# Performance work log

Hardware: AMD Instinct MI355X
Metric: run time of the kernel (lower is better)

## Reference

```python
import jax, jax.numpy as jnp
import numpy as np

B, N, P, K = 64, 64, 128, 16

def setup_inputs() -> dict:
    key = jax.random.key(0)
    k1, k2, k3, k4 = jax.random.split(key, 4)
    x = jax.random.normal(k1, (B, N, P), dtype=jnp.float32)
    idx = jax.random.randint(k2, (B, P), 0, K)
    x_mask = jax.nn.one_hot(idx, K, dtype=jnp.float32)  # [B, P, K] one-hot
    # xavier_normal_ init for weights [K, N*N]
    std = float(np.sqrt(2.0 / (K + N * N)))
    weights = std * jax.random.normal(k3, (K, N * N), dtype=jnp.float32)
    g = jax.random.uniform(k4, (N * N, N * N), dtype=jnp.float32)
    return {"x": x, "x_mask": x_mask, "weights": weights, "g": g}

def reference(x, x_mask, weights, g):
    b, n, p = x.shape
    wg = jnp.matmul(weights ** 2, g)               # [K, N*N]
    w = jnp.einsum('bpk,km->bpm', x_mask, wg)      # [B, P, N*N]
    ef = jnp.exp(-w.reshape(b, p, n, n))           # [B, P, N, N]
    # torch does x[b].reshape(p, -1, 1): row-major reinterpretation of [N,P] -> [P,N]
    xr = x.reshape(b, p, n)                        # [B, P, N]
    Z = jnp.einsum('bpij,bpj->bi', ef, xr)         # batched matvec, summed over p
    return (Z, w)
```

## Files before the change

### kernel.cpp

```cpp
#include <hip/hip_runtime.h>
#include <hip/hip_bf16.h>


__global__ __launch_bounds__(256) void k_gemm(const float* __restrict__ W,
                                              const float* __restrict__ G,
                                              float* __restrict__ part) {
    __shared__ float buf[8192];
    const int tc  = blockIdx.x & 15;
    const int mg  = blockIdx.x >> 4;
    const int tid = threadIdx.x;
    const int tt  = tid >> 4;
    const int col = tid & 15;
    const int t0  = tc * 256;

#pragma unroll
    for (int k = 0; k < 16; ++k) {
        float v = W[k * 4096 + t0 + tid];
        buf[k * 256 + tid] = v * v;
    }
    __syncthreads();

    const float4* G4 = (const float4*)G;
    const int mq = mg * 16 + col;

    float4 acc[16];
#pragma unroll
    for (int k = 0; k < 16; ++k) acc[k] = make_float4(0.f, 0.f, 0.f, 0.f);

#pragma unroll 8
    for (int i = 0; i < 16; ++i) {
        const int tl = tt * 16 + i;
        const float4 g4 = G4[(size_t)(t0 + tl) * 1024 + mq];
#pragma unroll
        for (int k = 0; k < 16; ++k) {
            const float s = buf[k * 256 + tl];
            acc[k].x = fmaf(s, g4.x, acc[k].x);
            acc[k].y = fmaf(s, g4.y, acc[k].y);
            acc[k].z = fmaf(s, g4.z, acc[k].z);
            acc[k].w = fmaf(s, g4.w, acc[k].w);
        }
    }
    __syncthreads();

    float4* red = (float4*)buf;
    float4* p4  = (float4*)part;
#pragma unroll
    for (int r = 0; r < 2; ++r) {
#pragma unroll
        for (int ks = 0; ks < 8; ++ks)
            red[ks * 256 + tid] = acc[r * 8 + ks];
        __syncthreads();
        if (tid < 128) {
            const int ks = tid >> 4;
            const int c2 = tid & 15;
            float4 s = make_float4(0.f, 0.f, 0.f, 0.f);
#pragma unroll
            for (int t2 = 0; t2 < 16; ++t2) {
                float4 v = red[ks * 256 + t2 * 16 + c2];
                s.x += v.x; s.y += v.y; s.z += v.z; s.w += v.w;
            }
            const int k = r * 8 + ks;
            p4[(size_t)tc * 16384 + (size_t)k * 1024 + mg * 16 + c2] = s;
        }
        __syncthreads();
    }
}

__global__ __launch_bounds__(256) void k_reduce(const float* __restrict__ part,
                                                float* __restrict__ wg,
                                                float* __restrict__ E) {
    const int q = blockIdx.x * 256 + threadIdx.x;
    const float4* p4 = (const float4*)part;
    float4 s = make_float4(0.f, 0.f, 0.f, 0.f);
#pragma unroll
    for (int tc = 0; tc < 16; ++tc) {
        float4 v = p4[(size_t)tc * 16384 + q];
        s.x += v.x; s.y += v.y; s.z += v.z; s.w += v.w;
    }
    ((float4*)wg)[q] = s;
    ((float4*)E)[q] = make_float4(expf(-s.x), expf(-s.y), expf(-s.z), expf(-s.w));
}

__global__ __launch_bounds__(256) void k_wz(const float* __restrict__ x,
                                            const float* __restrict__ xmask,
                                            const float* __restrict__ wg,
                                            const float* __restrict__ E,
                                            float* __restrict__ wout,
                                            float* __restrict__ zout) {
    __shared__ float sw[4][16][64];
    __shared__ int   idx[128];
    __shared__ float zr[16][16];
    const int tid = threadIdx.x;

    if (blockIdx.x < 8192) {
        const int bp = blockIdx.x;
        const float* xm = xmask + (size_t)bp * 16;
        int k = 0;
#pragma unroll
        for (int i = 0; i < 16; ++i) k = (xm[i] > 0.5f) ? i : k;
        const float4* src = (const float4*)(wg + (size_t)k * 4096);
        float4*       dst = (float4*)(wout + (size_t)bp * 4096);
#pragma unroll
        for (int c = 0; c < 4; ++c)
            dst[c * 256 + tid] = src[c * 256 + tid];
        return;
    }

    const int zb = blockIdx.x - 8192;
    const int b  = zb >> 2;
    const int iq = zb & 3;
    const int wv = tid >> 6;
    const int ln = tid & 63;

    if (tid < 128) {
        const float* xm = xmask + ((size_t)b * 128 + tid) * 16;
        int k = 0;
#pragma unroll
        for (int i = 0; i < 16; ++i) k = (xm[i] > 0.5f) ? i : k;
        idx[tid] = k;
    }
#pragma unroll
    for (int c = 0; c < 16; ++c)
        ((float*)sw)[c * 256 + tid] = 0.f;
    __syncthreads();

    const float* xb = x + (size_t)b * 8192;
    for (int p = wv * 32; p < wv * 32 + 32; ++p) {
        int k = idx[p];
        sw[wv][k][ln] += xb[p * 64 + ln];
    }
    __syncthreads();

    for (int e = tid; e < 1024; e += 256) {
        int k2 = e >> 6, j = e & 63;
        sw[0][k2][j] = sw[0][k2][j] + sw[1][k2][j] + sw[2][k2][j] + sw[3][k2][j];
    }
    __syncthreads();

    {
        const int k  = tid >> 4;
        const int il = tid & 15;
        const int i  = iq * 16 + il;
        float a = 0.f;
        const float4* Er = (const float4*)(E + (size_t)k * 4096 + i * 64);
        const float4* sr = (const float4*)(&sw[0][k][0]);
#pragma unroll
        for (int j4 = 0; j4 < 16; ++j4) {
            float4 e4 = Er[j4];
            float4 s4 = sr[j4];
            a = fmaf(e4.x, s4.x, a);
            a = fmaf(e4.y, s4.y, a);
            a = fmaf(e4.z, s4.z, a);
            a = fmaf(e4.w, s4.w, a);
        }
        zr[k][il] = a;
    }
    __syncthreads();
    if (tid < 16) {
        float s = 0.f;
#pragma unroll
        for (int k = 0; k < 16; ++k) s += zr[k][tid];
        zout[b * 64 + iq * 16 + tid] = s;
    }
}

extern "C" void kernel_launch(void* const* d_in, const int* in_sizes, int n_in,
                              void* d_out, int out_size, void* d_ws, size_t ws_size,
                              hipStream_t stream) {
    const float* x     = (const float*)d_in[0];
    const float* xmask = (const float*)d_in[1];
    const float* W     = (const float*)d_in[2];
    const float* G     = (const float*)d_in[3];

    float* zout = (float*)d_out;
    float* wout = (float*)d_out + 4096;

    float* wg = (float*)d_ws;
    float* E  = wg + 65536;

    float* part = wout;

    k_gemm  <<<1024, 256, 0, stream>>>(W, G, part);
    k_reduce<<<64,   256, 0, stream>>>(part, wg, E);
    k_wz    <<<8448, 256, 0, stream>>>(x, xmask, wg, E, wout, zout);
}
```

Before: 52.60 us.

## Double-buffer G tiles into LDS via direct global-to-LDS loads in GEMM

The GEMM kernel now streams each 16-row slice of G straight into LDS with the global_load_lds builtin, double-buffered so the next slice loads while the current one is consumed. The squared weights are stored transposed as float4 rows, so each thread reads four k-scales per LDS access instead of sixteen scalar loads. Row ownership changes from a contiguous 16-row chunk per thread group to an interleaved per-step row, which the later reduction still sums correctly. This adds a barrier every step and depends on the compiler inserting the wait for the async LDS writes before each barrier.

```diff
diff --git a/kernel.cpp b/kernel.cpp
--- a/kernel.cpp
+++ b/kernel.cpp
@@ -1,49 +1,79 @@
 #include <hip/hip_runtime.h>
 #include <hip/hip_bf16.h>
 
+
+__device__ __forceinline__ void dma16(const void* g, void* l) {
+    __builtin_amdgcn_global_load_lds(
+        (const __attribute__((address_space(1))) void*)g,
+        (__attribute__((address_space(3))) void*)l, 16, 0, 0);
+}
 
 __global__ __launch_bounds__(256) void k_gemm(const float* __restrict__ W,
                                               const float* __restrict__ G,
                                               float* __restrict__ part) {
     __shared__ float buf[8192];
+    float4* w2t4 = (float4*)buf;
+    float4* stg  = (float4*)(buf + 4096);
+
     const int tc  = blockIdx.x & 15;
     const int mg  = blockIdx.x >> 4;
     const int tid = threadIdx.x;
+    const int wv  = tid >> 6;
+    const int ln  = tid & 63;
     const int tt  = tid >> 4;
-    const int col = tid & 15;
     const int t0  = tc * 256;
 
-#pragma unroll
-    for (int k = 0; k < 16; ++k) {
-        float v = W[k * 4096 + t0 + tid];
-        buf[k * 256 + tid] = v * v;
-    }
-    __syncthreads();
+    {
+        float v[16];
+#pragma unroll
+        for (int k = 0; k < 16; ++k) {
+            float w = W[k * 4096 + t0 + tid];
+            v[k] = w * w;
+        }
+#pragma unroll
+        for (int q = 0; q < 4; ++q)
+            w2t4[tid * 4 + q] = make_float4(v[4*q], v[4*q+1], v[4*q+2], v[4*q+3]);
+    }
 
     const float4* G4 = (const float4*)G;
-    const int mq = mg * 16 + col;
+    const int fi  = wv * 64 + ln;
+    const int tl_ = fi >> 4;
+    const int mc_ = fi & 15;
+
+    dma16(&G4[(size_t)(t0 + tl_) * 1024 + mg * 16 + mc_], &stg[wv * 64]);
+    __syncthreads();
 
     float4 acc[16];
 #pragma unroll
     for (int k = 0; k < 16; ++k) acc[k] = make_float4(0.f, 0.f, 0.f, 0.f);
 
-#pragma unroll 8
-    for (int i = 0; i < 16; ++i) {
-        const int tl = tt * 16 + i;
-        const float4 g4 = G4[(size_t)(t0 + tl) * 1024 + mq];
-#pragma unroll
-        for (int k = 0; k < 16; ++k) {
-            const float s = buf[k * 256 + tl];
-            acc[k].x = fmaf(s, g4.x, acc[k].x);
-            acc[k].y = fmaf(s, g4.y, acc[k].y);
-            acc[k].z = fmaf(s, g4.z, acc[k].z);
-            acc[k].w = fmaf(s, g4.w, acc[k].w);
-        }
-    }
-    __syncthreads();
+    for (int s = 0; s < 16; ++s) {
+        if (s < 15)
+            dma16(&G4[(size_t)(t0 + (s + 1) * 16 + tl_) * 1024 + mg * 16 + mc_],
+                  &stg[((s + 1) & 1) * 256 + wv * 64]);
+
+        const float4 g4 = stg[(s & 1) * 256 + tid];
+        const float4* wr = &w2t4[(s * 16 + tt) * 4];
+#pragma unroll
+        for (int q = 0; q < 4; ++q) {
+            const float4 wq = wr[q];
+            const float* wf = (const float*)&wq;
+#pragma unroll
+            for (int c = 0; c < 4; ++c) {
+                const float sc = wf[c];
+                acc[q*4+c].x = fmaf(sc, g4.x, acc[q*4+c].x);
+                acc[q*4+c].y = fmaf(sc, g4.y, acc[q*4+c].y);
+                acc[q*4+c].z = fmaf(sc, g4.z, acc[q*4+c].z);
+                acc[q*4+c].w = fmaf(sc, g4.w, acc[q*4+c].w);
+            }
+        }
+        __syncthreads();
+    }
 
     float4* red = (float4*)buf;
     float4* p4  = (float4*)part;
+    const int col = tid & 15;
+    (void)col;
 #pragma unroll
     for (int r = 0; r < 2; ++r) {
 #pragma unroll
```

New measurement: 50.62 us. 3.8% less time.
